# Optimization experiments

Hardware: AMD Instinct MI355X
Metric: run time of the kernel (lower is better)

The kernel has to match this reference:

```python
import jax, jax.numpy as jnp
import numpy as np
import math

NUM_HEADS = 4


def setup_inputs() -> dict:
    key = jax.random.key(0)
    k1, k2, k3, k4 = jax.random.split(key, 4)
    b, c, f, t = 8, 512, 32, 64
    x = jax.random.normal(k1, (b, c, f, t), dtype=jnp.float32)
    # Conv1d(k=1) weights stored as 2D (out, in); fan-in scaled like torch default
    qkv_w = jax.random.normal(k2, (3 * c, c), dtype=jnp.float32) / math.sqrt(c)
    qkv_b = jax.random.normal(k3, (3 * c,), dtype=jnp.float32) * 0.02
    proj_w = jax.random.normal(k4, (c, c), dtype=jnp.float32) / math.sqrt(c)
    proj_b = jnp.zeros((c,), dtype=jnp.float32)
    return {"x": x, "qkv_w": qkv_w, "qkv_b": qkv_b, "proj_w": proj_w, "proj_b": proj_b}


def reference(x, qkv_w, qkv_b, proj_w, proj_b):
    b, c, f, t = x.shape
    T = f * t
    xr = x.reshape(b, c, T)  # [b, c, T]
    # Note: original forward computes PositionalEncoding2D(x) but discards it.
    qkv = jnp.einsum('oc,bct->bot', qkv_w, xr) + qkv_b[None, :, None]  # [b, 3c, T]
    H = NUM_HEADS
    ch = c // H
    q, k, v = jnp.split(qkv, 3, axis=1)  # each [b, c, T]
    q = q.reshape(b * H, ch, T)
    k = k.reshape(b * H, ch, T)
    v = v.reshape(b * H, ch, T)
    scale = 1.0 / math.sqrt(math.sqrt(ch))
    w = jnp.einsum('bct,bcs->bts', q * scale, k * scale)  # [b*H, T, T]
    w = jax.nn.softmax(w.astype(jnp.float32), axis=-1).astype(q.dtype)
    a = jnp.einsum('bts,bcs->bct', w, v).reshape(b, c, T)
    h = jnp.einsum('oc,bct->bot', proj_w, a) + proj_b[None, :, None]
    return (xr + h).reshape(b, c, f, t)
```

## Files before the change

### kernel.cpp

```cpp
#include <hip/hip_runtime.h>

#define DEV static __device__ __forceinline__

typedef __attribute__((ext_vector_type(8))) short short8;
typedef __attribute__((ext_vector_type(4))) float f32x4;
typedef __attribute__((ext_vector_type(16))) float f32x16;

DEV unsigned short f2bf(float f) {
    union { float f; unsigned int u; } v; v.f = f;
    unsigned int u = v.u;
    unsigned int r = (u + 0x7fffu + ((u >> 16) & 1u)) >> 16;
    return (unsigned short)r;
}

DEV unsigned int cvtpk(float lo, float hi) {
    unsigned int r;
    asm("v_cvt_pk_bf16_f32 %0, %1, %2" : "=v"(r) : "v"(lo), "v"(hi));
    return r;
}

DEV unsigned short* swp(unsigned short* base, int row, int col, int rs) {
    int a = ((row * rs + col) << 1) ^ ((row & 7) << 4);
    return (unsigned short*)((char*)base + a);
}

__global__ void prep_kernel(const float* __restrict__ qkv_w,
                            const float* __restrict__ proj_w,
                            unsigned short* __restrict__ Wq,
                            unsigned short* __restrict__ Wp) {
    int i = blockIdx.x * blockDim.x + threadIdx.x;
    int stride = gridDim.x * blockDim.x;
    for (int j = i; j < 1536 * 512; j += stride) Wq[j] = f2bf(qkv_w[j]);
    for (int j = i; j < 512 * 512;  j += stride) Wp[j] = f2bf(proj_w[j]);
}

__global__ __launch_bounds__(256) void transpose_kernel(const float* __restrict__ x,
                                                        unsigned short* __restrict__ Xt) {
    __shared__ unsigned char lt[64 * 128];
    int b  = blockIdx.z;
    int c0 = blockIdx.y * 64;
    int t0 = blockIdx.x * 64;
    int tid = threadIdx.x;
    int tx = tid & 15, cy0 = tid >> 4;
    for (int p = 0; p < 4; ++p) {
        int cy = cy0 + p * 16;
        const float* src = &x[((size_t)(b * 512 + c0 + cy)) * 2048 + t0 + tx * 4];
        f32x4 v = *(const f32x4*)src;
        unsigned long long pk = (unsigned long long)f2bf(v[0])
                              | ((unsigned long long)f2bf(v[1]) << 16)
                              | ((unsigned long long)f2bf(v[2]) << 32)
                              | ((unsigned long long)f2bf(v[3]) << 48);
        int addr = (cy * 128 + tx * 8) ^ ((cy & 7) << 4);
        *(unsigned long long*)(lt + addr) = pk;
    }
    __syncthreads();
    int c16 = (tid & 3) * 16, tr = tid >> 2;
    unsigned short buf[16];
    for (int i = 0; i < 16; ++i) {
        int c = c16 + i;
        int addr = (c * 128 + tr * 2) ^ ((c & 7) << 4);
        buf[i] = *(unsigned short*)(lt + addr);
    }
    unsigned short* dst = &Xt[((size_t)(b * 2048 + t0 + tr)) * 512 + c0 + c16];
    *(short8*)dst       = *(short8*)&buf[0];
    *(short8*)(dst + 8) = *(short8*)&buf[8];
}

#define LP 72

template <int ORIENT>
__global__ __launch_bounds__(256, 2) void gemm_qkv_kernel(
    const unsigned short* __restrict__ Wq,
    const unsigned short* __restrict__ Xt,
    const float* __restrict__ qkv_b,
    unsigned short* __restrict__ Qw,
    unsigned short* __restrict__ Kw,
    unsigned short* __restrict__ Vw) {
    __shared__ unsigned short Ws[128][LP];
    __shared__ unsigned short Bs[128][LP];
    int b  = blockIdx.z;
    int ot = (ORIENT == 0) ? blockIdx.y : (8 + blockIdx.y);
    int o0 = ot * 128, t0 = blockIdx.x * 128;
    int tid = threadIdx.x, lane = tid & 63, w = tid >> 6;
    int lr = lane >> 4, lc = lane & 15;
    int wr = (w >> 1) * 64, wc = (w & 1) * 64;
    f32x4 acc[4][4];
    for (int m = 0; m < 4; m++)
        for (int n = 0; n < 4; n++) acc[m][n] = (f32x4){0.f, 0.f, 0.f, 0.f};
    int srow = tid >> 3, soff = (tid & 7) * 8;
    for (int k0 = 0; k0 < 512; k0 += 64) {
        __syncthreads();
        for (int rr = srow; rr < 128; rr += 32) {
            *(short8*)&Ws[rr][soff] = *(const short8*)&Wq[(size_t)(o0 + rr) * 512 + k0 + soff];
            *(short8*)&Bs[rr][soff] = *(const short8*)&Xt[((size_t)(b * 2048) + t0 + rr) * 512 + k0 + soff];
        }
        __syncthreads();
        for (int kk = 0; kk < 64; kk += 32) {
            int kb = kk + lr * 8;
            short8 af[4], bfv[4];
            if (ORIENT == 0) {
                for (int m = 0; m < 4; m++) af[m]  = *(const short8*)&Bs[wr + m * 16 + lc][kb];
                for (int n = 0; n < 4; n++) bfv[n] = *(const short8*)&Ws[wc + n * 16 + lc][kb];
            } else {
                for (int m = 0; m < 4; m++) af[m]  = *(const short8*)&Ws[wr + m * 16 + lc][kb];
                for (int n = 0; n < 4; n++) bfv[n] = *(const short8*)&Bs[wc + n * 16 + lc][kb];
            }
            for (int m = 0; m < 4; m++)
                for (int n = 0; n < 4; n++)
                    acc[m][n] = __builtin_amdgcn_mfma_f32_16x16x32_bf16(af[m], bfv[n], acc[m][n], 0, 0, 0);
        }
    }
    const float scale = 0.29730177875068026f;
    for (int m = 0; m < 4; m++)
        for (int n = 0; n < 4; n++)
            for (int r = 0; r < 4; r++) {
                int row = wr + m * 16 + lr * 4 + r;
                int col = wc + n * 16 + lc;
                float val = acc[m][n][r];
                if (ORIENT == 0) {
                    int t = t0 + row;
                    int o = o0 + col;
                    val = (val + qkv_b[o]) * scale;
                    if (o < 512) {
                        int h = o >> 7, cc = o & 127;
                        Qw[((size_t)((b * 4 + h) * 2048 + t)) * 128 + cc] = f2bf(val);
                    } else {
                        int oo = o - 512;
                        int h = oo >> 7, cc = oo & 127;
                        Kw[((size_t)((b * 4 + h) * 2048 + t)) * 128 + cc] = f2bf(val);
                    }
                } else {
                    int o = o0 + row;
                    int t = t0 + col;
                    val += qkv_b[o];
                    int oo = o - 1024;
                    int h = oo >> 7, cc = oo & 127;
                    Vw[((size_t)((b * 4 + h) * 128 + cc)) * 2048 + t] = f2bf(val);
                }
            }
}

__global__ __launch_bounds__(512, 2) void attn_kernel(
    const unsigned short* __restrict__ Qw,
    const unsigned short* __restrict__ Kw,
    const unsigned short* __restrict__ Vw,
    unsigned short* __restrict__ Aw) {
    __shared__ unsigned short lds[32768];
    int bid = blockIdx.x;
    int bh = bid & 31;
    int t0 = (bid >> 5) * 256;
    int tid = threadIdx.x, lane = tid & 63, w = tid >> 6;
    int l31 = lane & 31, hi = lane >> 5;
    int qrow = w * 32;

    const unsigned short* Kbase = &Kw[(size_t)bh * 2048 * 128];
    const unsigned short* Vbase = &Vw[(size_t)bh * 128 * 2048];

    short8 qf[8];
    #pragma unroll
    for (int st = 0; st < 8; st++)
        qf[st] = *(const short8*)&Qw[((size_t)bh * 2048 + t0 + qrow + l31) * 128 + st * 16 + hi * 8];

    f32x16 oacc[4];
    #pragma unroll
    for (int ct = 0; ct < 4; ct++)
        #pragma unroll
        for (int i = 0; i < 16; i++) oacc[ct][i] = 0.f;
    float mst = -1e30f, lst = 0.f;

    int kr = tid >> 4, ko = (tid & 15) * 8;
    int vr = tid >> 3, vo = (tid & 7) * 8;

    short8 kreg[2], vreg[2];
    #pragma unroll
    for (int p = 0; p < 2; p++)
        kreg[p] = *(const short8*)&Kbase[(size_t)(kr + p * 32) * 128 + ko];
    #pragma unroll
    for (int p = 0; p < 2; p++)
        vreg[p] = *(const short8*)&Vbase[(size_t)(vr + p * 64) * 2048 + vo];

    for (int it = 0; it < 32; ++it) {
        int cur = it & 1;
        unsigned short* Kb = lds + cur * 8192;
        unsigned short* Vb = lds + 16384 + cur * 8192;
        #pragma unroll
        for (int p = 0; p < 2; p++) *(short8*)swp(Kb, kr + p * 32, ko, 128) = kreg[p];
        #pragma unroll
        for (int p = 0; p < 2; p++) *(short8*)swp(Vb, vr + p * 64, vo, 64) = vreg[p];
        if (it + 1 < 32) {
            int s1 = (it + 1) * 64;
            #pragma unroll
            for (int p = 0; p < 2; p++)
                kreg[p] = *(const short8*)&Kbase[(size_t)(s1 + kr + p * 32) * 128 + ko];
            #pragma unroll
            for (int p = 0; p < 2; p++)
                vreg[p] = *(const short8*)&Vbase[(size_t)(vr + p * 64) * 2048 + s1 + vo];
        }
        __syncthreads();

        f32x16 s0, s1v;
        #pragma unroll
        for (int i = 0; i < 16; i++) { s0[i] = 0.f; s1v[i] = 0.f; }
        __builtin_amdgcn_s_setprio(1);
        #pragma unroll
        for (int st = 0; st < 8; st++) {
            short8 k0 = *(const short8*)swp(Kb, l31,      st * 16 + hi * 8, 128);
            short8 k1 = *(const short8*)swp(Kb, 32 + l31, st * 16 + hi * 8, 128);
            s0  = __builtin_amdgcn_mfma_f32_32x32x16_bf16(k0, qf[st], s0, 0, 0, 0);
            s1v = __builtin_amdgcn_mfma_f32_32x32x16_bf16(k1, qf[st], s1v, 0, 0, 0);
        }
        __builtin_amdgcn_s_setprio(0);

        float m16[16];
        #pragma unroll
        for (int i = 0; i < 16; i++) m16[i] = fmaxf(s0[i], s1v[i]);
        #pragma unroll
        for (int sdt = 8; sdt > 0; sdt >>= 1)
            #pragma unroll
            for (int i = 0; i < 8; i++)
                if (i < sdt) m16[i] = fmaxf(m16[i], m16[i + sdt]);
        float mx = fmaxf(m16[0], __shfl_xor(m16[0], 32, 64));
        float mnew = fmaxf(mst, mx);
        float resc = __expf(mst - mnew);
        mst = mnew;
        float pe[32];
        #pragma unroll
        for (int i = 0; i < 16; i++) pe[i]      = __expf(s0[i]  - mnew);
        #pragma unroll
        for (int i = 0; i < 16; i++) pe[16 + i] = __expf(s1v[i] - mnew);
        float a16[16];
        #pragma unroll
        for (int i = 0; i < 16; i++) a16[i] = pe[i] + pe[16 + i];
        #pragma unroll
        for (int sdt = 8; sdt > 0; sdt >>= 1)
            #pragma unroll
            for (int i = 0; i < 8; i++)
                if (i < sdt) a16[i] = a16[i] + a16[i + sdt];
        float rs = a16[0] + __shfl_xor(a16[0], 32, 64);
        lst = lst * resc + rs;
        #pragma unroll
        for (int ct = 0; ct < 4; ct++)
            #pragma unroll
            for (int i = 0; i < 16; i++) oacc[ct][i] *= resc;

        short8 pf[4];
        #pragma unroll
        for (int st = 0; st < 4; st++) {
            unsigned X0 = cvtpk(pe[st * 8 + 0], pe[st * 8 + 1]);
            unsigned X1 = cvtpk(pe[st * 8 + 2], pe[st * 8 + 3]);
            unsigned Y0 = cvtpk(pe[st * 8 + 4], pe[st * 8 + 5]);
            unsigned Y1 = cvtpk(pe[st * 8 + 6], pe[st * 8 + 7]);
            unsigned Xp0 = (unsigned)__shfl_xor((int)X0, 32, 64);
            unsigned Xp1 = (unsigned)__shfl_xor((int)X1, 32, 64);
            unsigned Yp0 = (unsigned)__shfl_xor((int)Y0, 32, 64);
            unsigned Yp1 = (unsigned)__shfl_xor((int)Y1, 32, 64);
            union { unsigned u[4]; short8 s; } uu;
            uu.u[0] = hi ? Yp0 : X0;
            uu.u[1] = hi ? Yp1 : X1;
            uu.u[2] = hi ? Y0  : Xp0;
            uu.u[3] = hi ? Y1  : Xp1;
            pf[st] = uu.s;
        }

        __builtin_amdgcn_s_setprio(1);
        #pragma unroll
        for (int ct = 0; ct < 4; ct++)
            #pragma unroll
            for (int st = 0; st < 4; st++) {
                short8 va = *(const short8*)swp(Vb, ct * 32 + l31, st * 16 + hi * 8, 64);
                oacc[ct] = __builtin_amdgcn_mfma_f32_32x32x16_bf16(va, pf[st], oacc[ct], 0, 0, 0);
            }
        __builtin_amdgcn_s_setprio(0);
    }

    __syncthreads();
    unsigned short* ep = lds + w * 4096;
    float invl = 1.f / lst;
    #pragma unroll
    for (int ct = 0; ct < 4; ct++)
        #pragma unroll
        for (int i = 0; i < 8; i++) {
            int c = (2 * i & 3) + 8 * (i >> 1) + 4 * hi + 32 * ct;
            unsigned d = cvtpk(oacc[ct][2 * i] * invl, oacc[ct][2 * i + 1] * invl);
            *(unsigned*)swp(ep, l31, c, 128) = d;
        }
    asm volatile("" ::: "memory");
    int q = lane >> 1, hf = lane & 1;
    int b = bh >> 2, h = bh & 3;
    #pragma unroll
    for (int p = 0; p < 8; p++) {
        short8 v = *(const short8*)swp(ep, q, hf * 64 + p * 8, 128);
        *(short8*)&Aw[((size_t)(b * 2048) + t0 + qrow + q) * 512 + h * 128 + hf * 64 + p * 8] = v;
    }
}

__global__ __launch_bounds__(256, 2) void gemm_proj_kernel(
    const unsigned short* __restrict__ Wp,
    const unsigned short* __restrict__ Aw,
    const float* __restrict__ proj_b,
    const float* __restrict__ x,
    float* __restrict__ out) {
    __shared__ unsigned short Ws[128][LP];
    __shared__ unsigned short Bs[128][LP];
    int b  = blockIdx.z;
    int o0 = blockIdx.y * 128, t0 = blockIdx.x * 128;
    int tid = threadIdx.x, lane = tid & 63, w = tid >> 6;
    int lr = lane >> 4, lc = lane & 15;
    int wr = (w >> 1) * 64, wc = (w & 1) * 64;
    f32x4 acc[4][4];
    for (int m = 0; m < 4; m++)
        for (int n = 0; n < 4; n++) acc[m][n] = (f32x4){0.f, 0.f, 0.f, 0.f};
    int srow = tid >> 3, soff = (tid & 7) * 8;
    for (int k0 = 0; k0 < 512; k0 += 64) {
        __syncthreads();
        for (int rr = srow; rr < 128; rr += 32) {
            *(short8*)&Ws[rr][soff] = *(const short8*)&Wp[(size_t)(o0 + rr) * 512 + k0 + soff];
            *(short8*)&Bs[rr][soff] = *(const short8*)&Aw[((size_t)(b * 2048) + t0 + rr) * 512 + k0 + soff];
        }
        __syncthreads();
        for (int kk = 0; kk < 64; kk += 32) {
            int kb = kk + lr * 8;
            short8 af[4], bfv[4];
            for (int m = 0; m < 4; m++) af[m]  = *(const short8*)&Ws[wr + m * 16 + lc][kb];
            for (int n = 0; n < 4; n++) bfv[n] = *(const short8*)&Bs[wc + n * 16 + lc][kb];
            for (int m = 0; m < 4; m++)
                for (int n = 0; n < 4; n++)
                    acc[m][n] = __builtin_amdgcn_mfma_f32_16x16x32_bf16(af[m], bfv[n], acc[m][n], 0, 0, 0);
        }
    }
    for (int m = 0; m < 4; m++)
        for (int n = 0; n < 4; n++)
            for (int r = 0; r < 4; r++) {
                int o = o0 + wr + m * 16 + lr * 4 + r;
                int t = t0 + wc + n * 16 + lc;
                size_t idx = ((size_t)(b * 512) + o) * 2048 + t;
                out[idx] = x[idx] + acc[m][n][r] + proj_b[o];
            }
}

extern "C" void kernel_launch(void* const* d_in, const int* in_sizes, int n_in,
                              void* d_out, int out_size, void* d_ws, size_t ws_size,
                              hipStream_t stream) {
    const float* x      = (const float*)d_in[0];
    const float* qkv_w  = (const float*)d_in[1];
    const float* qkv_b  = (const float*)d_in[2];
    const float* proj_w = (const float*)d_in[3];
    const float* proj_b = (const float*)d_in[4];
    float* out = (float*)d_out;

    unsigned short* ws = (unsigned short*)d_ws;
    unsigned short* Wq = ws;
    unsigned short* Wp = Wq + (size_t)1536 * 512;
    unsigned short* Xt = Wp + (size_t)512 * 512;
    unsigned short* Qw = Xt + (size_t)8 * 2048 * 512;
    unsigned short* Kw = Qw + (size_t)32 * 2048 * 128;
    unsigned short* Vw = Kw + (size_t)32 * 2048 * 128;
    unsigned short* Aw = Vw + (size_t)32 * 2048 * 128;

    prep_kernel<<<dim3(512), dim3(256), 0, stream>>>(qkv_w, proj_w, Wq, Wp);
    transpose_kernel<<<dim3(32, 8, 8), dim3(256), 0, stream>>>(x, Xt);
    gemm_qkv_kernel<0><<<dim3(16, 8, 8), dim3(256), 0, stream>>>(Wq, Xt, qkv_b, Qw, Kw, Vw);
    gemm_qkv_kernel<1><<<dim3(16, 4, 8), dim3(256), 0, stream>>>(Wq, Xt, qkv_b, Qw, Kw, Vw);
    attn_kernel<<<dim3(256), dim3(512), 0, stream>>>(Qw, Kw, Vw, Aw);
    gemm_proj_kernel<<<dim3(16, 4, 8), dim3(256), 0, stream>>>(Wp, Aw, proj_b, x, out);
}
```

Before: 178.6 us.

## Process two query blocks per wave in attention, lazy rescale, permlane32 swaps

```diff
diff --git a/kernel.cpp b/kernel.cpp
--- a/kernel.cpp
+++ b/kernel.cpp
@@ -5,6 +5,7 @@
 typedef __attribute__((ext_vector_type(8))) short short8;
 typedef __attribute__((ext_vector_type(4))) float f32x4;
 typedef __attribute__((ext_vector_type(16))) float f32x16;
+typedef __attribute__((ext_vector_type(2))) unsigned int uint2v;
 
 DEV unsigned short f2bf(float f) {
     union { float f; unsigned int u; } v; v.f = f;
@@ -17,6 +18,19 @@
     unsigned int r;
     asm("v_cvt_pk_bf16_f32 %0, %1, %2" : "=v"(r) : "v"(lo), "v"(hi));
     return r;
+}
+
+DEV float pl32_max(float v) {
+    union { float f; unsigned u; } c; c.f = v;
+    uint2v r = __builtin_amdgcn_permlane32_swap(c.u, c.u, false, false);
+    union { unsigned u; float f; } a, b; a.u = r[0]; b.u = r[1];
+    return fmaxf(a.f, b.f);
+}
+DEV float pl32_sum(float v) {
+    union { float f; unsigned u; } c; c.f = v;
+    uint2v r = __builtin_amdgcn_permlane32_swap(c.u, c.u, false, false);
+    union { unsigned u; float f; } a, b; a.u = r[0]; b.u = r[1];
+    return a.f + b.f;
 }
 
 DEV unsigned short* swp(unsigned short* base, int row, int col, int rs) {
@@ -140,7 +154,7 @@
             }
 }
 
-__global__ __launch_bounds__(512, 2) void attn_kernel(
+__global__ __launch_bounds__(256, 1) void attn_kernel(
     const unsigned short* __restrict__ Qw,
     const unsigned short* __restrict__ Kw,
     const unsigned short* __restrict__ Vw,
@@ -151,115 +165,128 @@
     int t0 = (bid >> 5) * 256;
     int tid = threadIdx.x, lane = tid & 63, w = tid >> 6;
     int l31 = lane & 31, hi = lane >> 5;
-    int qrow = w * 32;
+    int qrow = w * 64;
 
     const unsigned short* Kbase = &Kw[(size_t)bh * 2048 * 128];
     const unsigned short* Vbase = &Vw[(size_t)bh * 128 * 2048];
 
-    short8 qf[8];
-    #pragma unroll
-    for (int st = 0; st < 8; st++)
-        qf[st] = *(const short8*)&Qw[((size_t)bh * 2048 + t0 + qrow + l31) * 128 + st * 16 + hi * 8];
-
-    f32x16 oacc[4];
-    #pragma unroll
-    for (int ct = 0; ct < 4; ct++)
-        #pragma unroll
-        for (int i = 0; i < 16; i++) oacc[ct][i] = 0.f;
-    float mst = -1e30f, lst = 0.f;
+    short8 qf[2][8];
+    #pragma unroll
+    for (int qb = 0; qb < 2; qb++)
+        #pragma unroll
+        for (int st = 0; st < 8; st++)
+            qf[qb][st] = *(const short8*)&Qw[((size_t)bh * 2048 + t0 + qrow + qb * 32 + l31) * 128 + st * 16 + hi * 8];
+
+    f32x16 oacc[2][4];
+    #pragma unroll
+    for (int qb = 0; qb < 2; qb++)
+        #pragma unroll
+        for (int ct = 0; ct < 4; ct++)
+            #pragma unroll
+            for (int i = 0; i < 16; i++) oacc[qb][ct][i] = 0.f;
+    float mst[2] = {-1e30f, -1e30f}, lst[2] = {0.f, 0.f};
 
     int kr = tid >> 4, ko = (tid & 15) * 8;
     int vr = tid >> 3, vo = (tid & 7) * 8;
 
-    short8 kreg[2], vreg[2];
-    #pragma unroll
-    for (int p = 0; p < 2; p++)
-        kreg[p] = *(const short8*)&Kbase[(size_t)(kr + p * 32) * 128 + ko];
-    #pragma unroll
-    for (int p = 0; p < 2; p++)
-        vreg[p] = *(const short8*)&Vbase[(size_t)(vr + p * 64) * 2048 + vo];
+    short8 kreg[4], vreg[4];
+    #pragma unroll
+    for (int p = 0; p < 4; p++)
+        kreg[p] = *(const short8*)&Kbase[(size_t)(kr + p * 16) * 128 + ko];
+    #pragma unroll
+    for (int p = 0; p < 4; p++)
+        vreg[p] = *(const short8*)&Vbase[(size_t)(vr + p * 32) * 2048 + vo];
 
     for (int it = 0; it < 32; ++it) {
         int cur = it & 1;
         unsigned short* Kb = lds + cur * 8192;
         unsigned short* Vb = lds + 16384 + cur * 8192;
         #pragma unroll
-        for (int p = 0; p < 2; p++) *(short8*)swp(Kb, kr + p * 32, ko, 128) = kreg[p];
-        #pragma unroll
-        for (int p = 0; p < 2; p++) *(short8*)swp(Vb, vr + p * 64, vo, 64) = vreg[p];
+        for (int p = 0; p < 4; p++) *(short8*)swp(Kb, kr + p * 16, ko, 128) = kreg[p];
+        #pragma unroll
+        for (int p = 0; p < 4; p++) *(short8*)swp(Vb, vr + p * 32, vo, 64) = vreg[p];
         if (it + 1 < 32) {
             int s1 = (it + 1) * 64;
             #pragma unroll
-            for (int p = 0; p < 2; p++)
-                kreg[p] = *(const short8*)&Kbase[(size_t)(s1 + kr + p * 32) * 128 + ko];
-            #pragma unroll
-            for (int p = 0; p < 2; p++)
-                vreg[p] = *(const short8*)&Vbase[(size_t)(vr + p * 64) * 2048 + s1 + vo];
-        }
-        __syncthreads();
-
-        f32x16 s0, s1v;
-        #pragma unroll
-        for (int i = 0; i < 16; i++) { s0[i] = 0.f; s1v[i] = 0.f; }
+            for (int p = 0; p < 4; p++)
+                kreg[p] = *(const short8*)&Kbase[(size_t)(s1 + kr + p * 16) * 128 + ko];
+            #pragma unroll
+            for (int p = 0; p < 4; p++)
+                vreg[p] = *(const short8*)&Vbase[(size_t)(vr + p * 32) * 2048 + s1 + vo];
+        }
+        __syncthreads();
+
+        f32x16 sacc[2][2];
+        #pragma unroll
+        for (int qb = 0; qb < 2; qb++)
+            #pragma unroll
+            for (int hh = 0; hh < 2; hh++)
+                #pragma unroll
+                for (int i = 0; i < 16; i++) sacc[qb][hh][i] = 0.f;
         __builtin_amdgcn_s_setprio(1);
         #pragma unroll
         for (int st = 0; st < 8; st++) {
             short8 k0 = *(const short8*)swp(Kb, l31,      st * 16 + hi * 8, 128);
             short8 k1 = *(const short8*)swp(Kb, 32 + l31, st * 16 + hi * 8, 128);
-            s0  = __builtin_amdgcn_mfma_f32_32x32x16_bf16(k0, qf[st], s0, 0, 0, 0);
-            s1v = __builtin_amdgcn_mfma_f32_32x32x16_bf16(k1, qf[st], s1v, 0, 0, 0);
+            sacc[0][0] = __builtin_amdgcn_mfma_f32_32x32x16_bf16(k0, qf[0][st], sacc[0][0], 0, 0, 0);
+            sacc[0][1] = __builtin_amdgcn_mfma_f32_32x32x16_bf16(k1, qf[0][st], sacc[0][1], 0, 0, 0);
+            sacc[1][0] = __builtin_amdgcn_mfma_f32_32x32x16_bf16(k0, qf[1][st], sacc[1][0], 0, 0, 0);
+            sacc[1][1] = __builtin_amdgcn_mfma_f32_32x32x16_bf16(k1, qf[1][st], sacc[1][1], 0, 0, 0);
         }
         __builtin_amdgcn_s_setprio(0);
 
-        float m16[16];
-        #pragma unroll
-        for (int i = 0; i < 16; i++) m16[i] = fmaxf(s0[i], s1v[i]);
-        #pragma unroll
-        for (int sdt = 8; sdt > 0; sdt >>= 1)
-            #pragma unroll
-            for (int i = 0; i < 8; i++)
-                if (i < sdt) m16[i] = fmaxf(m16[i], m16[i + sdt]);
-        float mx = fmaxf(m16[0], __shfl_xor(m16[0], 32, 64));
-        float mnew = fmaxf(mst, mx);
-        float resc = __expf(mst - mnew);
-        mst = mnew;
-        float pe[32];
-        #pragma unroll
-        for (int i = 0; i < 16; i++) pe[i]      = __expf(s0[i]  - mnew);
-        #pragma unroll
-        for (int i = 0; i < 16; i++) pe[16 + i] = __expf(s1v[i] - mnew);
-        float a16[16];
-        #pragma unroll
-        for (int i = 0; i < 16; i++) a16[i] = pe[i] + pe[16 + i];
-        #pragma unroll
-        for (int sdt = 8; sdt > 0; sdt >>= 1)
-            #pragma unroll
-            for (int i = 0; i < 8; i++)
-                if (i < sdt) a16[i] = a16[i] + a16[i + sdt];
-        float rs = a16[0] + __shfl_xor(a16[0], 32, 64);
-        lst = lst * resc + rs;
-        #pragma unroll
-        for (int ct = 0; ct < 4; ct++)
-            #pragma unroll
-            for (int i = 0; i < 16; i++) oacc[ct][i] *= resc;
-
-        short8 pf[4];
-        #pragma unroll
-        for (int st = 0; st < 4; st++) {
-            unsigned X0 = cvtpk(pe[st * 8 + 0], pe[st * 8 + 1]);
-            unsigned X1 = cvtpk(pe[st * 8 + 2], pe[st * 8 + 3]);
-            unsigned Y0 = cvtpk(pe[st * 8 + 4], pe[st * 8 + 5]);
-            unsigned Y1 = cvtpk(pe[st * 8 + 6], pe[st * 8 + 7]);
-            unsigned Xp0 = (unsigned)__shfl_xor((int)X0, 32, 64);
-            unsigned Xp1 = (unsigned)__shfl_xor((int)X1, 32, 64);
-            unsigned Yp0 = (unsigned)__shfl_xor((int)Y0, 32, 64);
-            unsigned Yp1 = (unsigned)__shfl_xor((int)Y1, 32, 64);
-            union { unsigned u[4]; short8 s; } uu;
-            uu.u[0] = hi ? Yp0 : X0;
-            uu.u[1] = hi ? Yp1 : X1;
-            uu.u[2] = hi ? Y0  : Xp0;
-            uu.u[3] = hi ? Y1  : Xp1;
-            pf[st] = uu.s;
+        short8 pf[2][4];
+        #pragma unroll
+        for (int qb = 0; qb < 2; qb++) {
+            float m16[16];
+            #pragma unroll
+            for (int i = 0; i < 16; i++) m16[i] = fmaxf(sacc[qb][0][i], sacc[qb][1][i]);
+            #pragma unroll
+            for (int sdt = 8; sdt > 0; sdt >>= 1)
+                #pragma unroll
+                for (int i = 0; i < 8; i++)
+                    if (i < sdt) m16[i] = fmaxf(m16[i], m16[i + sdt]);
+            float mx = pl32_max(m16[0]);
+            if (!__all(mx <= mst[qb] + 8.0f)) {
+                float mnew = fmaxf(mst[qb], mx);
+                float resc = __expf(mst[qb] - mnew);
+                mst[qb] = mnew;
+                lst[qb] *= resc;
+                #pragma unroll
+                for (int ct = 0; ct < 4; ct++)
+                    #pragma unroll
+                    for (int i = 0; i < 16; i++) oacc[qb][ct][i] *= resc;
+            }
+            float pe[32];
+            #pragma unroll
+            for (int i = 0; i < 16; i++) pe[i]      = __expf(sacc[qb][0][i] - mst[qb]);
+            #pragma unroll
+            for (int i = 0; i < 16; i++) pe[16 + i] = __expf(sacc[qb][1][i] - mst[qb]);
+            float a16[16];
+            #pragma unroll
+            for (int i = 0; i < 16; i++) a16[i] = pe[i] + pe[16 + i];
+            #pragma unroll
+            for (int sdt = 8; sdt > 0; sdt >>= 1)
+                #pragma unroll
+                for (int i = 0; i < 8; i++)
+                    if (i < sdt) a16[i] = a16[i] + a16[i + sdt];
+            lst[qb] += pl32_sum(a16[0]);
+
+            #pragma unroll
+            for (int st = 0; st < 4; st++) {
+                unsigned X0 = cvtpk(pe[st * 8 + 0], pe[st * 8 + 1]);
+                unsigned X1 = cvtpk(pe[st * 8 + 2], pe[st * 8 + 3]);
+                unsigned Y0 = cvtpk(pe[st * 8 + 4], pe[st * 8 + 5]);
+                unsigned Y1 = cvtpk(pe[st * 8 + 6], pe[st * 8 + 7]);
+                uint2v r0 = __builtin_amdgcn_permlane32_swap(X0, Y0, false, false);
+                uint2v r1 = __builtin_amdgcn_permlane32_swap(X1, Y1, false, false);
+                union { unsigned u[4]; short8 s; } uu;
+                uu.u[0] = r0[0];
+                uu.u[1] = r1[0];
+                uu.u[2] = r0[1];
+                uu.u[3] = r1[1];
+                pf[qb][st] = uu.s;
+            }
         }
 
         __builtin_amdgcn_s_setprio(1);
@@ -268,29 +295,34 @@
             #pragma unroll
             for (int st = 0; st < 4; st++) {
                 short8 va = *(const short8*)swp(Vb, ct * 32 + l31, st * 16 + hi * 8, 64);
-                oacc[ct] = __builtin_amdgcn_mfma_f32_32x32x16_bf16(va, pf[st], oacc[ct], 0, 0, 0);
+                oacc[0][ct] = __builtin_amdgcn_mfma_f32_32x32x16_bf16(va, pf[0][st], oacc[0][ct], 0, 0, 0);
+                oacc[1][ct] = __builtin_amdgcn_mfma_f32_32x32x16_bf16(va, pf[1][st], oacc[1][ct], 0, 0, 0);
             }
         __builtin_amdgcn_s_setprio(0);
     }
 
     __syncthreads();
     unsigned short* ep = lds + w * 4096;
-    float invl = 1.f / lst;
-    #pragma unroll
-    for (int ct = 0; ct < 4; ct++)
-        #pragma unroll
-        for (int i = 0; i < 8; i++) {
-            int c = (2 * i & 3) + 8 * (i >> 1) + 4 * hi + 32 * ct;
-            unsigned d = cvtpk(oacc[ct][2 * i] * invl, oacc[ct][2 * i + 1] * invl);
-            *(unsigned*)swp(ep, l31, c, 128) = d;
-        }
-    asm volatile("" ::: "memory");
+    int b = bh >> 2, h = bh & 3;
     int q = lane >> 1, hf = lane & 1;
-    int b = bh >> 2, h = bh & 3;
-    #pragma unroll
-    for (int p = 0; p < 8; p++) {
-        short8 v = *(const short8*)swp(ep, q, hf * 64 + p * 8, 128);
-        *(short8*)&Aw[((size_t)(b * 2048) + t0 + qrow + q) * 512 + h * 128 + hf * 64 + p * 8] = v;
+    #pragma unroll
+    for (int qb = 0; qb < 2; qb++) {
+        float invl = 1.f / lst[qb];
+        #pragma unroll
+        for (int ct = 0; ct < 4; ct++)
+            #pragma unroll
+            for (int i = 0; i < 8; i++) {
+                int c = (2 * i & 3) + 8 * (i >> 1) + 4 * hi + 32 * ct;
+                unsigned d = cvtpk(oacc[qb][ct][2 * i] * invl, oacc[qb][ct][2 * i + 1] * invl);
+                *(unsigned*)swp(ep, l31, c, 128) = d;
+            }
+        asm volatile("" ::: "memory");
+        #pragma unroll
+        for (int p = 0; p < 8; p++) {
+            short8 v = *(const short8*)swp(ep, q, hf * 64 + p * 8, 128);
+            *(short8*)&Aw[((size_t)(b * 2048) + t0 + qrow + qb * 32 + q) * 512 + h * 128 + hf * 64 + p * 8] = v;
+        }
+        asm volatile("" ::: "memory");
     }
 }
 
@@ -361,6 +393,6 @@
     transpose_kernel<<<dim3(32, 8, 8), dim3(256), 0, stream>>>(x, Xt);
     gemm_qkv_kernel<0><<<dim3(16, 8, 8), dim3(256), 0, stream>>>(Wq, Xt, qkv_b, Qw, Kw, Vw);
     gemm_qkv_kernel<1><<<dim3(16, 4, 8), dim3(256), 0, stream>>>(Wq, Xt, qkv_b, Qw, Kw, Vw);
-    attn_kernel<<<dim3(256), dim3(512), 0, stream>>>(Qw, Kw, Vw, Aw);
+    attn_kernel<<<dim3(256), dim3(256), 0, stream>>>(Qw, Kw, Vw, Aw);
     gemm_proj_kernel<<<dim3(16, 4, 8), dim3(256), 0, stream>>>(Wp, Aw, proj_b, x, out);
 }
```

Measured after the change: 188.0 us. 1.05x slower.
